# Optimization experiments

Measured on AMD Instinct MI355X. Metric: run time of the kernel, lower is better.

Reference implementation:

```python
import jax, jax.numpy as jnp
import numpy as np

T, B, DIM, N = 2048, 16, 1024, 64


def setup_inputs() -> dict:
    key = jax.random.key(0)
    ks = jax.random.split(key, 6)
    # xavier-uniform-ish scale for [N, DIM] linear weights
    lim = float(np.sqrt(6.0 / (DIM + N)))
    mk = lambda k: jax.random.uniform(k, (N, DIM), jnp.float32, -lim, lim)
    return {
        "x": jax.random.normal(ks[0], (T, B, DIM), jnp.float32),
        "S": jnp.zeros((B, N, N), jnp.float32),
        "W_k": mk(ks[1]),
        "W_v": mk(ks[2]),
        "W_q": mk(ks[3]),
        "W_alpha": mk(ks[4]),
        "d_alpha": jnp.full((N,), 0.1, jnp.float32),
        "b_alpha": jnp.full((N,), 2.0, jnp.float32),
    }


def reference(x, S, W_k, W_v, W_q, W_alpha, d_alpha, b_alpha):
    # Projections for the whole sequence at once: [T, B, N]
    k_all = jnp.einsum('tbd,nd->tbn', x, W_k)
    v_all = jnp.einsum('tbd,nd->tbn', x, W_v)
    q_all = jnp.einsum('tbd,nd->tbn', x, W_q)
    a_all = jnp.einsum('tbd,nd->tbn', x, W_alpha)

    def step(S, inp):
        k, v, q, ax = inp  # each [B, N]
        retrieved = jnp.einsum('bij,bj->bi', S, k)                 # [B, N]
        alpha = jax.nn.sigmoid(ax + d_alpha * retrieved + b_alpha)  # [B, N]
        outer_vk = v[:, :, None] * k[:, None, :]                    # [B, N, N]
        S = alpha[:, :, None] * S + (1.0 - alpha[:, :, None]) * outer_vk
        out = jnp.einsum('bij,bj->bi', S, q)                        # [B, N]
        out = out * jax.nn.silu(out)
        return S, out

    S_final, output = jax.lax.scan(step, S, (k_all, v_all, q_all, a_all))
    return output, S_final
```

## Files before the change

kernel.cpp:

```cpp
#include <hip/hip_runtime.h>
#include <hip/hip_bf16.h>

#define T_STEPS 2048
#define BATCH 16
#define DIM 1024
#define NDIM 64
#define M_TOTAL (T_STEPS * BATCH)
#define STRIDE (BATCH * NDIM)
#define CH 32

typedef __attribute__((ext_vector_type(8))) short bf16x8;
typedef __attribute__((ext_vector_type(4))) float f32x4;
typedef __attribute__((ext_vector_type(2))) float f32x2;

__device__ inline unsigned pk_bf(float lo, float hi) {
    __hip_bfloat162 h = __float22bfloat162_rn(float2{lo, hi});
    return *(unsigned*)&h;
}

template <int CTRL>
__device__ inline float dpp_add(float x) {
    int v = __builtin_amdgcn_update_dpp(0, __float_as_int(x), CTRL, 0xF, 0xF, true);
    return x + __int_as_float(v);
}
__device__ inline float red16(float x) {
    x = dpp_add<0xB1>(x);
    x = dpp_add<0x4E>(x);
    x = dpp_add<0x141>(x);
    x = dpp_add<0x140>(x);
    return x;
}
__device__ inline float fast_sigmoid(float z) {
    return __builtin_amdgcn_rcpf(1.f + __expf(-z));
}

#define AS1 __attribute__((address_space(1)))
#define AS3 __attribute__((address_space(3)))
__device__ inline void gl_lds16(const float* g, float* l) {
    __builtin_amdgcn_global_load_lds((const AS1 unsigned*)g, (AS3 unsigned*)l, 16, 0, 0);
}
__device__ inline void gl_lds16s(const unsigned short* g, unsigned short* l) {
    __builtin_amdgcn_global_load_lds((const AS1 unsigned*)g, (AS3 unsigned*)l, 16, 0, 0);
}
__device__ inline void gl_lds4(const float* g, float* l) {
    __builtin_amdgcn_global_load_lds((const AS1 unsigned*)g, (AS3 unsigned*)l, 4, 0, 0);
}
#define WAIT_VM0 do { __builtin_amdgcn_s_waitcnt(0x0F70); asm volatile("" ::: "memory"); } while (0)

__global__ __launch_bounds__(256) void pack_w(
    const float* __restrict__ Wk, const float* __restrict__ Wq,
    const float* __restrict__ Wv, const float* __restrict__ Wa,
    unsigned short* __restrict__ Wb) {
    int n = blockIdx.x;
    int sel = n >> 6;
    const float* W = (sel == 0) ? Wk : (sel == 1) ? Wq : (sel == 2) ? Wv : Wa;
    int k4 = threadIdx.x * 4;
    float4 f = *(const float4*)(W + (size_t)(n & 63) * DIM + k4);
    uint2 u;
    u.x = pk_bf(f.x, f.y);
    u.y = pk_bf(f.z, f.w);
    *(uint2*)(Wb + (size_t)n * DIM + k4) = u;
}

__global__ __launch_bounds__(256, 2) void proj_kernel(
    const float* __restrict__ x, const unsigned short* __restrict__ Wb,
    const float* __restrict__ ba, float* __restrict__ Kp, float* __restrict__ Qp,
    float* __restrict__ VAi) {
    __shared__ float sA[128 * 64];
    __shared__ unsigned short sB[128 * 64];

    const int m0 = blockIdx.x * 128;
    const int ntile = blockIdx.y;
    const int tid = threadIdx.x;
    const int wv = tid >> 6, lane = tid & 63, lrow = lane & 15, quad = lane >> 4;
    const int wm = wv & 1, wn = wv >> 1;

    f32x4 acc[4][4];
#pragma unroll
    for (int a = 0; a < 4; a++)
#pragma unroll
        for (int b = 0; b < 4; b++) acc[a][b] = (f32x4)(0.f);

    const float* xg = x + (size_t)(m0 + (tid >> 4)) * DIM + (tid & 15) * 4;
    const unsigned short* wg = Wb + (size_t)(ntile * 128 + (tid >> 3)) * DIM + (tid & 7) * 8;

    for (int it = 0; it < 16; ++it) {
        const int k0 = it * 64;
        __syncthreads();
#pragma unroll
        for (int j = 0; j < 8; ++j)
            gl_lds16(xg + (size_t)(16 * j) * DIM + k0, &sA[(tid + 256 * j) * 4]);
#pragma unroll
        for (int j = 0; j < 4; ++j)
            gl_lds16s(wg + (size_t)(32 * j) * DIM + k0, &sB[(tid + 256 * j) * 8]);
        WAIT_VM0;
        __syncthreads();

#pragma unroll
        for (int ks = 0; ks < 2; ++ks) {
            bf16x8 af[4];
#pragma unroll
            for (int mt = 0; mt < 4; ++mt) {
                const float* pa = &sA[(wm * 64 + mt * 16 + lrow) * 64 + ks * 32 + quad * 8];
                float4 lo = ((const float4*)pa)[0], hi = ((const float4*)pa)[1];
                unsigned pk[4] = {pk_bf(lo.x, lo.y), pk_bf(lo.z, lo.w),
                                  pk_bf(hi.x, hi.y), pk_bf(hi.z, hi.w)};
                af[mt] = *(bf16x8*)pk;
            }
#pragma unroll
            for (int nt = 0; nt < 4; ++nt) {
                bf16x8 bfr = *(const bf16x8*)&sB[(wn * 64 + nt * 16 + lrow) * 64 + ks * 32 + quad * 8];
#pragma unroll
                for (int mt = 0; mt < 4; ++mt)
                    acc[mt][nt] = __builtin_amdgcn_mfma_f32_16x16x32_bf16(af[mt], bfr, acc[mt][nt], 0, 0, 0);
            }
        }
    }

    const int g2 = ntile * 2 + wn;
    float bav[4];
    if (g2 == 3) {
#pragma unroll
        for (int nt = 0; nt < 4; ++nt) bav[nt] = ba[nt * 16 + lrow];
    }
#pragma unroll
    for (int mt = 0; mt < 4; ++mt)
#pragma unroll
        for (int nt = 0; nt < 4; ++nt) {
            int col = nt * 16 + lrow;
#pragma unroll
            for (int reg = 0; reg < 4; ++reg) {
                int m = m0 + wm * 64 + mt * 16 + quad * 4 + reg;
                float vvv = acc[mt][nt][reg];
                if (g2 == 0) Kp[(size_t)m * 64 + col] = vvv;
                else if (g2 == 1) Qp[(size_t)m * 64 + col] = vvv;
                else if (g2 == 2) VAi[(size_t)m * 128 + col * 2] = vvv;
                else VAi[(size_t)m * 128 + col * 2 + 1] = vvv + bav[nt];
            }
        }
}

__global__ __launch_bounds__(256) void kq_kernel(
    const float* __restrict__ Kp, const float* __restrict__ Qp, float* __restrict__ kq) {
    int m = blockIdx.x * 16 + (threadIdx.x >> 4);
    int c = threadIdx.x & 15;
    float4 k = *(const float4*)(Kp + (size_t)m * 64 + c * 4);
    float4 q = *(const float4*)(Qp + (size_t)m * 64 + c * 4);
    float p = k.x * q.x + k.y * q.y + k.z * q.z + k.w * q.w;
    p = red16(p);
    if (c == 0) kq[m] = p;
}

__global__ __launch_bounds__(64, 1) void recur_kernel(
    const float* __restrict__ Kp, const float* __restrict__ Qp,
    const float* __restrict__ VAi, const float* __restrict__ KQp,
    const float* __restrict__ S0, const float* __restrict__ d_alpha,
    float* __restrict__ out, float* __restrict__ Sout) {
    __shared__ float Kl[2][CH][64];
    __shared__ float Ql[2][CH][64];
    __shared__ float VAl[2][CH][8];
    __shared__ float KQl[2][64];
    __shared__ float Ol[CH][4];

    int b = blockIdx.y, g = blockIdx.x, lane = threadIdx.x;
    int r = lane >> 4, c = lane & 15, i = g * 4 + r, c4 = c * 4;

    float4 sv = *(const float4*)(S0 + ((size_t)b * NDIM + i) * NDIM + c4);
    f32x2 s01 = {sv.x, sv.y}, s23 = {sv.z, sv.w};
    float da = d_alpha[i];

    const float* Kbase = Kp + (size_t)b * NDIM + (size_t)(lane >> 4) * STRIDE + (lane & 15) * 4;
    const float* Qbase = Qp + (size_t)b * NDIM + (size_t)(lane >> 4) * STRIDE + (lane & 15) * 4;
    const float* VAbase = VAi + (size_t)b * 128 + g * 8 + (lane & 1) * 4 + (size_t)(lane >> 1) * 2048;
    const float* KQbase = KQp + b + (size_t)(lane & 31) * BATCH;

    auto load_chunk = [&](int t0, int buf) {
#pragma unroll
        for (int j = 0; j < 8; ++j) {
            gl_lds16(Kbase + (size_t)(t0 + j * 4) * STRIDE, &Kl[buf][j * 4][0]);
            gl_lds16(Qbase + (size_t)(t0 + j * 4) * STRIDE, &Ql[buf][j * 4][0]);
        }
        gl_lds16(VAbase + (size_t)t0 * 2048, &VAl[buf][0][0]);
        gl_lds4(KQbase + (size_t)t0 * BATCH, &KQl[buf][0]);
    };

    load_chunk(0, 0);
    WAIT_VM0;

    f32x2 k01[2], k23[2], q01[2], q23[2], va[2];
    float kqv[2];
    {
        const float* Kb = &Kl[0][0][0];
        const float* Qb = &Ql[0][0][0];
#pragma unroll
        for (int u = 0; u < 2; ++u) {
            f32x4 kk = *(const f32x4*)(Kb + u * 64 + c4);
            f32x4 qq = *(const f32x4*)(Qb + u * 64 + c4);
            k01[u] = kk.lo; k23[u] = kk.hi;
            q01[u] = qq.lo; q23[u] = qq.hi;
            va[u] = *(const f32x2*)&VAl[0][u][r * 2];
            kqv[u] = KQl[0][u];
        }
    }

    for (int j = 0; j < T_STEPS / CH; ++j) {
        int cb = j & 1;
        if (j + 1 < T_STEPS / CH) load_chunk((j + 1) * CH, cb ^ 1);

        const float* Kb = &Kl[cb][0][0];
        const float* Qb = &Ql[cb][0][0];
        const float* Vb = &VAl[cb][0][0];
        const float* Qk = &KQl[cb][0];

#pragma unroll
        for (int tl = 0; tl < CH; ++tl) {
            int sl = tl & 1;
            f32x2 k0v = k01[sl], k1v = k23[sl], q0v = q01[sl], q1v = q23[sl];
            f32x2 vva = va[sl];
            float kq = kqv[sl];
            if (tl < CH - 2) {
                f32x4 kk = *(const f32x4*)(Kb + (tl + 2) * 64 + c4);
                f32x4 qq = *(const f32x4*)(Qb + (tl + 2) * 64 + c4);
                k01[sl] = kk.lo; k23[sl] = kk.hi;
                q01[sl] = qq.lo; q23[sl] = qq.hi;
                va[sl] = *(const f32x2*)&Vb[(tl + 2) * 8 + r * 2];
                kqv[sl] = Qk[tl + 2];
            }

            f32x2 pk_ = k0v * s01;
            pk_ = k1v * s23 + pk_;
            f32x2 pq_ = q0v * s01;
            pq_ = q1v * s23 + pq_;
            float rk = red16(pk_.x + pk_.y);
            float rq = red16(pq_.x + pq_.y);

            float v = vva.x;
            f32x2 w01 = v * k0v, w23 = v * k1v;
            f32x2 d01 = s01 - w01, d23 = s23 - w23;

            float alpha = fast_sigmoid(fmaf(da, rk, vva.y));
            f32x2 a2 = {alpha, alpha};
            s01 = w01 + a2 * d01;
            s23 = w23 + a2 * d23;

            float u1 = (1.f - alpha) * v;
            float o = fmaf(alpha, rq, u1 * kq);
            float ov = o * o * fast_sigmoid(o);
            if (c == 0) Ol[tl][r] = ov;
        }
        WAIT_VM0;

        if (lane < 32) {
            float4 t4 = *(const float4*)&Ol[lane][0];
            *(float4*)(out + ((size_t)(j * CH + lane) * BATCH + b) * NDIM + g * 4) = t4;
        }

        if (j + 1 < T_STEPS / CH) {
            int nb = cb ^ 1;
            const float* Kn = &Kl[nb][0][0];
            const float* Qn = &Ql[nb][0][0];
#pragma unroll
            for (int u = 0; u < 2; ++u) {
                f32x4 kk = *(const f32x4*)(Kn + u * 64 + c4);
                f32x4 qq = *(const f32x4*)(Qn + u * 64 + c4);
                k01[u] = kk.lo; k23[u] = kk.hi;
                q01[u] = qq.lo; q23[u] = qq.hi;
                va[u] = *(const f32x2*)&VAl[nb][u][r * 2];
                kqv[u] = KQl[nb][u];
            }
        }
    }

    float* so = Sout + ((size_t)b * NDIM + i) * NDIM + c4;
    *(float4*)so = float4{s01.x, s01.y, s23.x, s23.y};
}

extern "C" void kernel_launch(void* const* d_in, const int* in_sizes, int n_in,
                              void* d_out, int out_size, void* d_ws, size_t ws_size,
                              hipStream_t stream) {
    const float* x  = (const float*)d_in[0];
    const float* S0 = (const float*)d_in[1];
    const float* Wk = (const float*)d_in[2];
    const float* Wv = (const float*)d_in[3];
    const float* Wq = (const float*)d_in[4];
    const float* Wa = (const float*)d_in[5];
    const float* da = (const float*)d_in[6];
    const float* ba = (const float*)d_in[7];

    float* out = (float*)d_out;
    float* Sout = out + (size_t)T_STEPS * BATCH * NDIM;

    const size_t per = (size_t)M_TOTAL * NDIM;
    float* Kp  = (float*)d_ws;
    float* Qp  = Kp + per;
    float* VAi = Qp + per;
    float* kq  = VAi + 2 * per;
    unsigned short* Wb = (unsigned short*)(kq + M_TOTAL);

    pack_w<<<dim3(256), dim3(256), 0, stream>>>(Wk, Wq, Wv, Wa, Wb);
    proj_kernel<<<dim3(M_TOTAL / 128, 2), dim3(256), 0, stream>>>(x, Wb, ba, Kp, Qp, VAi);
    kq_kernel<<<dim3(M_TOTAL / 16), dim3(256), 0, stream>>>(Kp, Qp, kq);
    recur_kernel<<<dim3(16, BATCH), dim3(64), 0, stream>>>(Kp, Qp, VAi, kq, S0, da, out, Sout);
}
```

Before: 493.8 us.

## Compute next-step retrieval algebraically to shorten the serial recurrence dependency chain

The recurrence now computes the next step's retrieval S_{t+1}k_{t+1} from S_t·k_{t+1} and a precomputed k_t·k_{t+1} dot product, using the closed-form update rk = alpha*(ck - v*kk) + v*kk. This takes one cross-lane reduction off the critical path between the sigmoid and the state update, so the reduction can overlap with the previous step. The sigmoid argument is also prescaled by -log2(e) in the projection and in d_alpha, so alpha becomes a bare exp2 plus reciprocal. In exchange the projection kernel does an extra neighbour dot product, the recurrence keeps a third K buffer with one extra global load per chunk, and rounding behaviour changes slightly.

```diff
diff --git a/kernel.cpp b/kernel.cpp
--- a/kernel.cpp
+++ b/kernel.cpp
@@ -12,6 +12,8 @@
 typedef __attribute__((ext_vector_type(8))) short bf16x8;
 typedef __attribute__((ext_vector_type(4))) float f32x4;
 typedef __attribute__((ext_vector_type(2))) float f32x2;
+
+#define NEG_LOG2E -1.44269504088896f
 
 __device__ inline unsigned pk_bf(float lo, float hi) {
     __hip_bfloat162 h = __float22bfloat162_rn(float2{lo, hi});
@@ -135,31 +137,38 @@
                 if (g2 == 0) Kp[(size_t)m * 64 + col] = vvv;
                 else if (g2 == 1) Qp[(size_t)m * 64 + col] = vvv;
                 else if (g2 == 2) VAi[(size_t)m * 128 + col * 2] = vvv;
-                else VAi[(size_t)m * 128 + col * 2 + 1] = vvv + bav[nt];
+                else VAi[(size_t)m * 128 + col * 2 + 1] = NEG_LOG2E * (vvv + bav[nt]);
             }
         }
 }
 
 __global__ __launch_bounds__(256) void kq_kernel(
-    const float* __restrict__ Kp, const float* __restrict__ Qp, float* __restrict__ kq) {
+    const float* __restrict__ Kp, const float* __restrict__ Qp,
+    float* __restrict__ kq, float* __restrict__ kk) {
     int m = blockIdx.x * 16 + (threadIdx.x >> 4);
     int c = threadIdx.x & 15;
     float4 k = *(const float4*)(Kp + (size_t)m * 64 + c * 4);
     float4 q = *(const float4*)(Qp + (size_t)m * 64 + c * 4);
-    float p = k.x * q.x + k.y * q.y + k.z * q.z + k.w * q.w;
-    p = red16(p);
-    if (c == 0) kq[m] = p;
+    float4 kn = {0.f, 0.f, 0.f, 0.f};
+    if (m + BATCH < M_TOTAL) kn = *(const float4*)(Kp + (size_t)(m + BATCH) * 64 + c * 4);
+    float pq = k.x * q.x + k.y * q.y + k.z * q.z + k.w * q.w;
+    float pk = k.x * kn.x + k.y * kn.y + k.z * kn.z + k.w * kn.w;
+    pq = red16(pq);
+    pk = red16(pk);
+    if (c == 0) { kq[m] = pq; kk[m] = pk; }
 }
 
 __global__ __launch_bounds__(64, 1) void recur_kernel(
     const float* __restrict__ Kp, const float* __restrict__ Qp,
     const float* __restrict__ VAi, const float* __restrict__ KQp,
+    const float* __restrict__ KKp,
     const float* __restrict__ S0, const float* __restrict__ d_alpha,
     float* __restrict__ out, float* __restrict__ Sout) {
     __shared__ float Kl[2][CH][64];
     __shared__ float Ql[2][CH][64];
     __shared__ float VAl[2][CH][8];
     __shared__ float KQl[2][64];
+    __shared__ float KKl[2][64];
     __shared__ float Ol[CH][4];
 
     int b = blockIdx.y, g = blockIdx.x, lane = threadIdx.x;
@@ -167,12 +176,14 @@
 
     float4 sv = *(const float4*)(S0 + ((size_t)b * NDIM + i) * NDIM + c4);
     f32x2 s01 = {sv.x, sv.y}, s23 = {sv.z, sv.w};
-    float da = d_alpha[i];
+    float da2 = d_alpha[i] * NEG_LOG2E;
 
     const float* Kbase = Kp + (size_t)b * NDIM + (size_t)(lane >> 4) * STRIDE + (lane & 15) * 4;
     const float* Qbase = Qp + (size_t)b * NDIM + (size_t)(lane >> 4) * STRIDE + (lane & 15) * 4;
     const float* VAbase = VAi + (size_t)b * 128 + g * 8 + (lane & 1) * 4 + (size_t)(lane >> 1) * 2048;
     const float* KQbase = KQp + b + (size_t)(lane & 31) * BATCH;
+    const float* KKbase = KKp + b + (size_t)(lane & 31) * BATCH;
+    const float* Kgl = Kp + (size_t)b * NDIM + c4;
 
     auto load_chunk = [&](int t0, int buf) {
 #pragma unroll
@@ -182,71 +193,88 @@
         }
         gl_lds16(VAbase + (size_t)t0 * 2048, &VAl[buf][0][0]);
         gl_lds4(KQbase + (size_t)t0 * BATCH, &KQl[buf][0]);
+        gl_lds4(KKbase + (size_t)t0 * BATCH, &KKl[buf][0]);
     };
 
     load_chunk(0, 0);
     WAIT_VM0;
 
-    f32x2 k01[2], k23[2], q01[2], q23[2], va[2];
-    float kqv[2];
+    f32x2 kc01, kc23, kn01[2], kn23[2], q01[2], q23[2], va[2];
+    float kqv[2], kkv[2], rk;
     {
-        const float* Kb = &Kl[0][0][0];
-        const float* Qb = &Ql[0][0][0];
+        const float* Kb0 = &Kl[0][0][0];
+        const float* Qb0 = &Ql[0][0][0];
+        f32x4 k0 = *(const f32x4*)(Kb0 + c4);
+        kc01 = k0.lo; kc23 = k0.hi;
 #pragma unroll
         for (int u = 0; u < 2; ++u) {
-            f32x4 kk = *(const f32x4*)(Kb + u * 64 + c4);
-            f32x4 qq = *(const f32x4*)(Qb + u * 64 + c4);
-            k01[u] = kk.lo; k23[u] = kk.hi;
+            f32x4 kk_ = *(const f32x4*)(Kb0 + (u + 1) * 64 + c4);
+            kn01[u] = kk_.lo; kn23[u] = kk_.hi;
+            f32x4 qq = *(const f32x4*)(Qb0 + u * 64 + c4);
             q01[u] = qq.lo; q23[u] = qq.hi;
             va[u] = *(const f32x2*)&VAl[0][u][r * 2];
             kqv[u] = KQl[0][u];
-        }
+            kkv[u] = KKl[0][u];
+        }
+        f32x2 p = kc01 * s01;
+        p = kc23 * s23 + p;
+        rk = red16(p.x + p.y);
     }
 
     for (int j = 0; j < T_STEPS / CH; ++j) {
         int cb = j & 1;
         if (j + 1 < T_STEPS / CH) load_chunk((j + 1) * CH, cb ^ 1);
+        f32x4 kb = *(const f32x4*)(Kgl + (size_t)((j + 1) * CH) * STRIDE);
 
         const float* Kb = &Kl[cb][0][0];
         const float* Qb = &Ql[cb][0][0];
         const float* Vb = &VAl[cb][0][0];
         const float* Qk = &KQl[cb][0];
+        const float* Kk = &KKl[cb][0];
 
 #pragma unroll
         for (int tl = 0; tl < CH; ++tl) {
             int sl = tl & 1;
-            f32x2 k0v = k01[sl], k1v = k23[sl], q0v = q01[sl], q1v = q23[sl];
+            f32x2 knA = kn01[sl], knB = kn23[sl];
+            f32x2 q0v = q01[sl], q1v = q23[sl];
             f32x2 vva = va[sl];
-            float kq = kqv[sl];
+            float kqs = kqv[sl], kks = kkv[sl];
             if (tl < CH - 2) {
-                f32x4 kk = *(const f32x4*)(Kb + (tl + 2) * 64 + c4);
                 f32x4 qq = *(const f32x4*)(Qb + (tl + 2) * 64 + c4);
-                k01[sl] = kk.lo; k23[sl] = kk.hi;
                 q01[sl] = qq.lo; q23[sl] = qq.hi;
                 va[sl] = *(const f32x2*)&Vb[(tl + 2) * 8 + r * 2];
                 kqv[sl] = Qk[tl + 2];
-            }
-
-            f32x2 pk_ = k0v * s01;
-            pk_ = k1v * s23 + pk_;
-            f32x2 pq_ = q0v * s01;
-            pq_ = q1v * s23 + pq_;
-            float rk = red16(pk_.x + pk_.y);
+                kkv[sl] = Kk[tl + 2];
+            }
+            if (tl < CH - 3) {
+                f32x4 kk_ = *(const f32x4*)(Kb + (tl + 3) * 64 + c4);
+                kn01[sl] = kk_.lo; kn23[sl] = kk_.hi;
+            } else if (tl == CH - 3) {
+                kn01[sl] = kb.lo; kn23[sl] = kb.hi;
+            }
+
+            f32x2 pq_ = q0v * s01; pq_ = q1v * s23 + pq_;
+            f32x2 pk_ = knA * s01; pk_ = knB * s23 + pk_;
             float rq = red16(pq_.x + pq_.y);
+            float ck = red16(pk_.x + pk_.y);
 
             float v = vva.x;
-            f32x2 w01 = v * k0v, w23 = v * k1v;
+            f32x2 w01 = v * kc01, w23 = v * kc23;
             f32x2 d01 = s01 - w01, d23 = s23 - w23;
-
-            float alpha = fast_sigmoid(fmaf(da, rk, vva.y));
+            float vkk = v * kks, vkq = v * kqs;
+            float ckm = ck - vkk, rqm = rq - vkq;
+
+            float alpha = __builtin_amdgcn_rcpf(1.f + __builtin_amdgcn_exp2f(fmaf(da2, rk, vva.y)));
+            rk = fmaf(alpha, ckm, vkk);
+
             f32x2 a2 = {alpha, alpha};
             s01 = w01 + a2 * d01;
             s23 = w23 + a2 * d23;
 
-            float u1 = (1.f - alpha) * v;
-            float o = fmaf(alpha, rq, u1 * kq);
+            float o = fmaf(alpha, rqm, vkq);
             float ov = o * o * fast_sigmoid(o);
             if (c == 0) Ol[tl][r] = ov;
+            kc01 = knA; kc23 = knB;
         }
         WAIT_VM0;
 
@@ -261,12 +289,13 @@
             const float* Qn = &Ql[nb][0][0];
 #pragma unroll
             for (int u = 0; u < 2; ++u) {
-                f32x4 kk = *(const f32x4*)(Kn + u * 64 + c4);
+                f32x4 kk_ = *(const f32x4*)(Kn + (u + 1) * 64 + c4);
+                kn01[u] = kk_.lo; kn23[u] = kk_.hi;
                 f32x4 qq = *(const f32x4*)(Qn + u * 64 + c4);
-                k01[u] = kk.lo; k23[u] = kk.hi;
                 q01[u] = qq.lo; q23[u] = qq.hi;
                 va[u] = *(const f32x2*)&VAl[nb][u][r * 2];
                 kqv[u] = KQl[nb][u];
+                kkv[u] = KKl[nb][u];
             }
         }
     }
@@ -295,10 +324,11 @@
     float* Qp  = Kp + per;
     float* VAi = Qp + per;
     float* kq  = VAi + 2 * per;
-    unsigned short* Wb = (unsigned short*)(kq + M_TOTAL);
+    float* kk  = kq + M_TOTAL;
+    unsigned short* Wb = (unsigned short*)(kk + M_TOTAL);
 
     pack_w<<<dim3(256), dim3(256), 0, stream>>>(Wk, Wq, Wv, Wa, Wb);
     proj_kernel<<<dim3(M_TOTAL / 128, 2), dim3(256), 0, stream>>>(x, Wb, ba, Kp, Qp, VAi);
-    kq_kernel<<<dim3(M_TOTAL / 16), dim3(256), 0, stream>>>(Kp, Qp, kq);
-    recur_kernel<<<dim3(16, BATCH), dim3(64), 0, stream>>>(Kp, Qp, VAi, kq, S0, da, out, Sout);
-}
+    kq_kernel<<<dim3(M_TOTAL / 16), dim3(256), 0, stream>>>(Kp, Qp, kq, kk);
+    recur_kernel<<<dim3(16, BATCH), dim3(64), 0, stream>>>(Kp, Qp, VAi, kq, kk, S0, da, out, Sout);
+}
```

New measurement: 501.6 us. About the same (+1.6%).

## Fold log2e into alpha inputs and move output SiLU out of the recurrence

Applied to the files above, without the earlier changes.

The alpha bias projection and d_alpha are pre-scaled by -log2(e), so the per-step sigmoid uses a raw exp2 instead of expf. The output gating o*silu(o) moves from the serial recurrence into a separate elementwise kernel, which shortens each step's instruction stream. The two DPP reductions are interleaved so they can overlap, and the 32-step unrolled inner loop becomes a non-unrolled loop over a 4-step macro body. In exchange the change adds an extra kernel launch with a full read-write pass over the output. It also adds prefetch reads past the end of each chunk into adjacent shared memory, whose values are discarded.

```diff
diff --git a/kernel.cpp b/kernel.cpp
--- a/kernel.cpp
+++ b/kernel.cpp
@@ -13,6 +13,8 @@
 typedef __attribute__((ext_vector_type(4))) float f32x4;
 typedef __attribute__((ext_vector_type(2))) float f32x2;
 
+#define NEG_LOG2E -1.44269504088896f
+
 __device__ inline unsigned pk_bf(float lo, float hi) {
     __hip_bfloat162 h = __float22bfloat162_rn(float2{lo, hi});
     return *(unsigned*)&h;
@@ -30,8 +32,11 @@
     x = dpp_add<0x140>(x);
     return x;
 }
-__device__ inline float fast_sigmoid(float z) {
-    return __builtin_amdgcn_rcpf(1.f + __expf(-z));
+__device__ inline void red16x2(float& a, float& b) {
+    a = dpp_add<0xB1>(a);  b = dpp_add<0xB1>(b);
+    a = dpp_add<0x4E>(a);  b = dpp_add<0x4E>(b);
+    a = dpp_add<0x141>(a); b = dpp_add<0x141>(b);
+    a = dpp_add<0x140>(a); b = dpp_add<0x140>(b);
 }
 
 #define AS1 __attribute__((address_space(1)))
@@ -135,7 +140,7 @@
                 if (g2 == 0) Kp[(size_t)m * 64 + col] = vvv;
                 else if (g2 == 1) Qp[(size_t)m * 64 + col] = vvv;
                 else if (g2 == 2) VAi[(size_t)m * 128 + col * 2] = vvv;
-                else VAi[(size_t)m * 128 + col * 2 + 1] = vvv + bav[nt];
+                else VAi[(size_t)m * 128 + col * 2 + 1] = NEG_LOG2E * (vvv + bav[nt]);
             }
         }
 }
@@ -149,6 +154,18 @@
     float p = k.x * q.x + k.y * q.y + k.z * q.z + k.w * q.w;
     p = red16(p);
     if (c == 0) kq[m] = p;
+}
+
+__global__ __launch_bounds__(256) void silu_kernel(float* __restrict__ out) {
+    size_t idx = ((size_t)blockIdx.x * 256 + threadIdx.x) * 4;
+    f32x4 o = *(const f32x4*)(out + idx);
+    f32x4 rr;
+#pragma unroll
+    for (int j = 0; j < 4; ++j) {
+        float e = __builtin_amdgcn_exp2f(o[j] * NEG_LOG2E);
+        rr[j] = o[j] * o[j] * __builtin_amdgcn_rcpf(1.f + e);
+    }
+    *(f32x4*)(out + idx) = rr;
 }
 
 __global__ __launch_bounds__(64, 1) void recur_kernel(
@@ -167,7 +184,7 @@
 
     float4 sv = *(const float4*)(S0 + ((size_t)b * NDIM + i) * NDIM + c4);
     f32x2 s01 = {sv.x, sv.y}, s23 = {sv.z, sv.w};
-    float da = d_alpha[i];
+    float da2 = d_alpha[i] * NEG_LOG2E;
 
     const float* Kbase = Kp + (size_t)b * NDIM + (size_t)(lane >> 4) * STRIDE + (lane & 15) * 4;
     const float* Qbase = Qp + (size_t)b * NDIM + (size_t)(lane >> 4) * STRIDE + (lane & 15) * 4;
@@ -190,89 +207,91 @@
     f32x2 k01[2], k23[2], q01[2], q23[2], va[2];
     float kqv[2];
     {
-        const float* Kb = &Kl[0][0][0];
-        const float* Qb = &Ql[0][0][0];
+        const float* Kb0 = &Kl[0][0][0] + c4;
+        const float* Qb0 = &Ql[0][0][0] + c4;
 #pragma unroll
         for (int u = 0; u < 2; ++u) {
-            f32x4 kk = *(const f32x4*)(Kb + u * 64 + c4);
-            f32x4 qq = *(const f32x4*)(Qb + u * 64 + c4);
-            k01[u] = kk.lo; k23[u] = kk.hi;
-            q01[u] = qq.lo; q23[u] = qq.hi;
+            f32x4 kk_ = *(const f32x4*)(Kb0 + u * 64);
+            f32x4 qq_ = *(const f32x4*)(Qb0 + u * 64);
+            k01[u] = kk_.lo; k23[u] = kk_.hi;
+            q01[u] = qq_.lo; q23[u] = qq_.hi;
             va[u] = *(const f32x2*)&VAl[0][u][r * 2];
             kqv[u] = KQl[0][u];
         }
     }
 
+#define STEP(u, sl) do {                                                        \
+    f32x2 k0v = k01[sl], k1v = k23[sl], q0v = q01[sl], q1v = q23[sl];           \
+    f32x2 vva = va[sl];                                                         \
+    float kqs = kqv[sl];                                                        \
+    f32x4 kk_ = *(const f32x4*)(Kt + (u + 2) * 64);                             \
+    f32x4 qq_ = *(const f32x4*)(Qt + (u + 2) * 64);                             \
+    k01[sl] = kk_.lo; k23[sl] = kk_.hi;                                         \
+    q01[sl] = qq_.lo; q23[sl] = qq_.hi;                                         \
+    va[sl] = *(const f32x2*)(Vt + (u + 2) * 8);                                 \
+    kqv[sl] = Qk[t4 + u + 2];                                                   \
+    f32x2 pk_ = k0v * s01; pk_ = k1v * s23 + pk_;                               \
+    f32x2 pq_ = q0v * s01; pq_ = q1v * s23 + pq_;                               \
+    float rk_ = pk_.x + pk_.y, rq_ = pq_.x + pq_.y;                             \
+    red16x2(rk_, rq_);                                                          \
+    float v_ = vva.x;                                                           \
+    f32x2 w01 = v_ * k0v, w23 = v_ * k1v;                                       \
+    f32x2 d01 = s01 - w01, d23 = s23 - w23;                                     \
+    float alpha_ = __builtin_amdgcn_rcpf(                                       \
+        1.f + __builtin_amdgcn_exp2f(fmaf(da2, rk_, vva.y)));                   \
+    f32x2 a2 = {alpha_, alpha_};                                                \
+    s01 = w01 + a2 * d01;                                                       \
+    s23 = w23 + a2 * d23;                                                       \
+    float vkq_ = v_ * kqs;                                                      \
+    float o_ = fmaf(alpha_, rq_ - vkq_, vkq_);                     \
+    if (c == 0) Ol[t4 + u][r] = o_;                                             \
+} while (0)
+
+#pragma unroll 1
     for (int j = 0; j < T_STEPS / CH; ++j) {
-        int cb = j & 1;
-        if (j + 1 < T_STEPS / CH) load_chunk((j + 1) * CH, cb ^ 1);
-
-        const float* Kb = &Kl[cb][0][0];
-        const float* Qb = &Ql[cb][0][0];
-        const float* Vb = &VAl[cb][0][0];
+        const int cb = j & 1, nb = cb ^ 1;
+        if (j + 1 < T_STEPS / CH) load_chunk((j + 1) * CH, nb);
+
+        const float* Kb = &Kl[cb][0][0] + c4;
+        const float* Qb = &Ql[cb][0][0] + c4;
+        const float* Vb = &VAl[cb][0][0] + r * 2;
         const float* Qk = &KQl[cb][0];
 
-#pragma unroll
-        for (int tl = 0; tl < CH; ++tl) {
-            int sl = tl & 1;
-            f32x2 k0v = k01[sl], k1v = k23[sl], q0v = q01[sl], q1v = q23[sl];
-            f32x2 vva = va[sl];
-            float kq = kqv[sl];
-            if (tl < CH - 2) {
-                f32x4 kk = *(const f32x4*)(Kb + (tl + 2) * 64 + c4);
-                f32x4 qq = *(const f32x4*)(Qb + (tl + 2) * 64 + c4);
-                k01[sl] = kk.lo; k23[sl] = kk.hi;
-                q01[sl] = qq.lo; q23[sl] = qq.hi;
-                va[sl] = *(const f32x2*)&Vb[(tl + 2) * 8 + r * 2];
-                kqv[sl] = Qk[tl + 2];
-            }
-
-            f32x2 pk_ = k0v * s01;
-            pk_ = k1v * s23 + pk_;
-            f32x2 pq_ = q0v * s01;
-            pq_ = q1v * s23 + pq_;
-            float rk = red16(pk_.x + pk_.y);
-            float rq = red16(pq_.x + pq_.y);
-
-            float v = vva.x;
-            f32x2 w01 = v * k0v, w23 = v * k1v;
-            f32x2 d01 = s01 - w01, d23 = s23 - w23;
-
-            float alpha = fast_sigmoid(fmaf(da, rk, vva.y));
-            f32x2 a2 = {alpha, alpha};
-            s01 = w01 + a2 * d01;
-            s23 = w23 + a2 * d23;
-
-            float u1 = (1.f - alpha) * v;
-            float o = fmaf(alpha, rq, u1 * kq);
-            float ov = o * o * fast_sigmoid(o);
-            if (c == 0) Ol[tl][r] = ov;
+#pragma unroll 1
+        for (int t4 = 0; t4 < CH; t4 += 4) {
+            const float* Kt = Kb + t4 * 64;
+            const float* Qt = Qb + t4 * 64;
+            const float* Vt = Vb + t4 * 8;
+            STEP(0, 0);
+            STEP(1, 1);
+            STEP(2, 0);
+            STEP(3, 1);
         }
         WAIT_VM0;
 
         if (lane < 32) {
-            float4 t4 = *(const float4*)&Ol[lane][0];
-            *(float4*)(out + ((size_t)(j * CH + lane) * BATCH + b) * NDIM + g * 4) = t4;
+            float4 t4o = *(const float4*)&Ol[lane][0];
+            *(float4*)(out + ((size_t)(j * CH + lane) * BATCH + b) * NDIM + g * 4) = t4o;
         }
 
         if (j + 1 < T_STEPS / CH) {
-            int nb = cb ^ 1;
-            const float* Kn = &Kl[nb][0][0];
-            const float* Qn = &Ql[nb][0][0];
+            const float* Kn = &Kl[nb][0][0] + c4;
+            const float* Qn = &Ql[nb][0][0] + c4;
 #pragma unroll
             for (int u = 0; u < 2; ++u) {
-                f32x4 kk = *(const f32x4*)(Kn + u * 64 + c4);
-                f32x4 qq = *(const f32x4*)(Qn + u * 64 + c4);
-                k01[u] = kk.lo; k23[u] = kk.hi;
-                q01[u] = qq.lo; q23[u] = qq.hi;
+                f32x4 kk_ = *(const f32x4*)(Kn + u * 64);
+                f32x4 qq_ = *(const f32x4*)(Qn + u * 64);
+                k01[u] = kk_.lo; k23[u] = kk_.hi;
+                q01[u] = qq_.lo; q23[u] = qq_.hi;
                 va[u] = *(const f32x2*)&VAl[nb][u][r * 2];
                 kqv[u] = KQl[nb][u];
             }
         }
     }
-
-    float* so = Sout + ((size_t)b * NDIM + i) * NDIM + c4;
-    *(float4*)so = float4{s01.x, s01.y, s23.x, s23.y};
+#undef STEP
+
+    float* so_ = Sout + ((size_t)b * NDIM + i) * NDIM + c4;
+    *(float4*)so_ = float4{s01.x, s01.y, s23.x, s23.y};
 }
 
 extern "C" void kernel_launch(void* const* d_in, const int* in_sizes, int n_in,
@@ -301,4 +320,5 @@
     proj_kernel<<<dim3(M_TOTAL / 128, 2), dim3(256), 0, stream>>>(x, Wb, ba, Kp, Qp, VAi);
     kq_kernel<<<dim3(M_TOTAL / 16), dim3(256), 0, stream>>>(Kp, Qp, kq);
     recur_kernel<<<dim3(16, BATCH), dim3(64), 0, stream>>>(Kp, Qp, VAi, kq, S0, da, out, Sout);
-}
+    silu_kernel<<<dim3((T_STEPS * BATCH * NDIM) / (256 * 4)), dim3(256), 0, stream>>>(out);
+}
```

Measured after the change: 507.5 us. 1.03x slower.
